# Performance work log

Measured on AMD Instinct MI355X. Metric: run time of the kernel, lower is better.

## Reference

```python
import jax, jax.numpy as jnp
import numpy as np

N_NODES = 100000
IN_DIM = 128
N_EDGES = 600000
HIDDEN = 128


def setup_inputs() -> dict:
    key = jax.random.key(0)
    k_z, k_e, k_w1, k_b1, k_w2, k_b2 = jax.random.split(key, 6)
    z = jax.random.normal(k_z, (N_NODES, IN_DIM), dtype=jnp.float32)
    edge_index = jax.random.randint(k_e, (2, N_EDGES), 0, N_NODES, dtype=jnp.int64)
    # torch.nn.Linear weights: W has shape (out, in), y = x @ W.T + b
    lim1 = 1.0 / np.sqrt(2 * IN_DIM)
    W1 = jax.random.uniform(k_w1, (HIDDEN, 2 * IN_DIM), jnp.float32, -lim1, lim1)
    b1 = jax.random.uniform(k_b1, (HIDDEN,), jnp.float32, -lim1, lim1)
    lim2 = 1.0 / np.sqrt(HIDDEN)
    W2 = jax.random.uniform(k_w2, (1, HIDDEN), jnp.float32, -lim2, lim2)
    b2 = jax.random.uniform(k_b2, (1,), jnp.float32, -lim2, lim2)
    return {"z": z, "edge_index": edge_index, "W1": W1, "b1": b1, "W2": W2, "b2": b2}


def reference(z, edge_index, W1, b1, W2, b2):
    src, dst = edge_index[0], edge_index[1]
    pair = jnp.concatenate([z[src], z[dst]], axis=1)        # [E, 2*in_dim]
    h = jax.nn.relu(pair @ W1.T + b1)                        # [E, 128]
    out = (h @ W2.T + b2).squeeze(-1)                        # [E]
    return out
```

## Files before the change

kernel.cpp:

```cpp
#include <hip/hip_runtime.h>

#define IN_DIM 128
#define NCOL   256

typedef __bf16 bfx8 __attribute__((ext_vector_type(8)));
typedef __bf16 bfx4 __attribute__((ext_vector_type(4)));
typedef float  f32x4 __attribute__((ext_vector_type(4)));

__device__ __forceinline__ int swz(int x) { return x ^ (((x >> 9) & 7) << 4); }

__global__ __launch_bounds__(256, 2) void gemm_mfma(
    const float* __restrict__ z, const float* __restrict__ W1,
    const float* __restrict__ b1, __bf16* __restrict__ UV, int nchunks)
{
    __shared__ float abuf[2][32 * IN_DIM];

    const int tid  = threadIdx.x;
    const int wave = tid >> 6;
    const int lane = tid & 63;
    const int l15  = lane & 15;
    const int q    = lane >> 4;
    const int n0   = wave * 64;

    bfx8  bfrag[4][4];
    f32x4 bias[4];
#pragma unroll
    for (int nt = 0; nt < 4; ++nt) {
        const int n = n0 + nt * 16 + l15;
        const float* src = (n < 128) ? (W1 + (size_t)n * 256)
                                     : (W1 + (size_t)(n - 128) * 256 + 128);
#pragma unroll
        for (int kk = 0; kk < 4; ++kk) {
            float4 f0 = *(const float4*)(src + kk * 32 + q * 8);
            float4 f1 = *(const float4*)(src + kk * 32 + q * 8 + 4);
            bfx8 b;
            b[0]=(__bf16)f0.x; b[1]=(__bf16)f0.y; b[2]=(__bf16)f0.z; b[3]=(__bf16)f0.w;
            b[4]=(__bf16)f1.x; b[5]=(__bf16)f1.y; b[6]=(__bf16)f1.z; b[7]=(__bf16)f1.w;
            bfrag[nt][kk] = b;
        }
        if (n0 + nt * 16 < 128) bias[nt] = *(const f32x4*)(b1 + n0 + nt * 16 + q * 4);
        else                    bias[nt] = (f32x4){0.f, 0.f, 0.f, 0.f};
    }

    auto STAGE = [&](int b, int cc) {
        const char* gbase = (const char*)(z + (size_t)cc * 32 * IN_DIM);
#pragma unroll
        for (int i = 0; i < 4; ++i) {
            const int seg  = (wave * 4 + i) << 10;
            const int loff = seg + lane * 16;
            __builtin_amdgcn_global_load_lds(
                (const __attribute__((address_space(1))) void*)(gbase + swz(loff)),
                (__attribute__((address_space(3))) void*)((char*)&abuf[b][0] + seg),
                16, 0, 0);
        }
    };

    int c = blockIdx.x;
    STAGE(0, c);
    __syncthreads();
    int cur = 0;

    for (; c < nchunks; c += gridDim.x) {
        const int cn = c + gridDim.x;
        if (cn < nchunks) STAGE(cur ^ 1, cn);

        const char* tb = (const char*)&abuf[cur][0];
        const int m0 = c * 32;

        f32x4 acc[2][4];
#pragma unroll
        for (int mt = 0; mt < 2; ++mt)
#pragma unroll
            for (int nt = 0; nt < 4; ++nt)
                acc[mt][nt] = (f32x4){0.f, 0.f, 0.f, 0.f};

#pragma unroll
        for (int kk = 0; kk < 4; ++kk) {
            bfx8 af[2];
#pragma unroll
            for (int mt = 0; mt < 2; ++mt) {
                const int r = mt * 16 + l15;
                const int o = r * 512 + kk * 128 + q * 32;
                f32x4 f0 = *(const f32x4*)(tb + swz(o));
                f32x4 f1 = *(const f32x4*)(tb + swz(o + 16));
                bfx8 a;
                a[0]=(__bf16)f0[0]; a[1]=(__bf16)f0[1]; a[2]=(__bf16)f0[2]; a[3]=(__bf16)f0[3];
                a[4]=(__bf16)f1[0]; a[5]=(__bf16)f1[1]; a[6]=(__bf16)f1[2]; a[7]=(__bf16)f1[3];
                af[mt] = a;
            }
#pragma unroll
            for (int mt = 0; mt < 2; ++mt)
#pragma unroll
                for (int nt = 0; nt < 4; ++nt)
                    acc[mt][nt] = __builtin_amdgcn_mfma_f32_16x16x32_bf16(
                        bfrag[nt][kk], af[mt], acc[mt][nt], 0, 0, 0);
        }

#pragma unroll
        for (int mt = 0; mt < 2; ++mt) {
            __bf16* dst = UV + (size_t)(m0 + mt * 16 + l15) * NCOL + n0 + q * 4;
#pragma unroll
            for (int nt = 0; nt < 4; ++nt) {
                bfx4 v;
#pragma unroll
                for (int r = 0; r < 4; ++r)
                    v[r] = (__bf16)(acc[mt][nt][r] + bias[nt][r]);
                *(bfx4*)(dst + nt * 16) = v;
            }
        }

        __syncthreads();
        cur ^= 1;
    }
}

__global__ __launch_bounds__(256) void edge_mlp(
    const __bf16* __restrict__ UV, const int* __restrict__ ei,
    const float* __restrict__ W2, const float* __restrict__ b2,
    float* __restrict__ out, int E)
{
    const int gt   = blockIdx.x * blockDim.x + threadIdx.x;
    const int lane = threadIdx.x & 15;
    const int g    = gt >> 4;
    const int e0   = g * 2;
    const int j0   = lane * 8;

    float ww[8];
    {
        float4 w0 = *(const float4*)(W2 + j0);
        float4 w1 = *(const float4*)(W2 + j0 + 4);
        ww[0] = w0.x; ww[1] = w0.y; ww[2] = w0.z; ww[3] = w0.w;
        ww[4] = w1.x; ww[5] = w1.y; ww[6] = w1.z; ww[7] = w1.w;
    }

    if (e0 >= E) return;

    const int2 srcp = *(const int2*)(ei + e0);
    const int2 dstp = *(const int2*)(ei + E + e0);

    bfx8 u0 = *(const bfx8*)(UV + (size_t)srcp.x * NCOL + j0);
    bfx8 v0 = *(const bfx8*)(UV + (size_t)dstp.x * NCOL + 128 + j0);
    bfx8 u1 = *(const bfx8*)(UV + (size_t)srcp.y * NCOL + j0);
    bfx8 v1 = *(const bfx8*)(UV + (size_t)dstp.y * NCOL + 128 + j0);

    float s0 = 0.f, s1 = 0.f;
#pragma unroll
    for (int i = 0; i < 8; ++i) {
        float h0 = (float)u0[i] + (float)v0[i];
        float h1 = (float)u1[i] + (float)v1[i];
        s0 = fmaf(fmaxf(h0, 0.f), ww[i], s0);
        s1 = fmaf(fmaxf(h1, 0.f), ww[i], s1);
    }

#pragma unroll
    for (int d = 1; d < 16; d <<= 1) {
        s0 += __shfl_xor(s0, d);
        s1 += __shfl_xor(s1, d);
    }

    if (lane == 0) {
        float bb = b2[0];
        *(float2*)(out + e0) = make_float2(s0 + bb, s1 + bb);
    }
}

extern "C" void kernel_launch(void* const* d_in, const int* in_sizes, int n_in,
                              void* d_out, int out_size, void* d_ws, size_t ws_size,
                              hipStream_t stream)
{
    const float* z  = (const float*)d_in[0];
    const int*   ei = (const int*)d_in[1];
    const float* W1 = (const float*)d_in[2];
    const float* b1 = (const float*)d_in[3];
    const float* W2 = (const float*)d_in[4];
    const float* b2 = (const float*)d_in[5];
    float* out = (float*)d_out;

    const int M = in_sizes[0] / IN_DIM;
    const int E = in_sizes[1] / 2;

    __bf16* UV = (__bf16*)d_ws;

    const int nchunks = M / 32;
    gemm_mfma<<<512, 256, 0, stream>>>(z, W1, b1, UV, nchunks);

    int groups  = (E + 1) / 2;
    int eblocks = (groups * 16 + 255) / 256;
    edge_mlp<<<eblocks, 256, 0, stream>>>(UV, ei, W2, b2, out, E);
}
```

Measured before the change: 154.4 us.

## Deepen GEMM LDS pipeline to four stages with explicit vmcnt waits

Raises the z-tile staging ring from double to quadruple buffering (three chunks in flight) and swaps __syncthreads for manual s_waitcnt vmcnt counts plus raw s_barrier, so compute waits only on the chunk it needs. LDS reads move to inline ds_read_b128 asm issued together before the MFMA loop. LDS use doubles to 64KB per block, which may limit occupancy at two blocks per CU. The hand-counted vmcnt values are fragile because they also count the UV global stores.

Result: no change. 151.5 us (-1.9%).

```diff
diff --git a/kernel.cpp b/kernel.cpp
--- a/kernel.cpp
+++ b/kernel.cpp
@@ -1,11 +1,14 @@
 #include <hip/hip_runtime.h>
+#include <stdint.h>
 
 #define IN_DIM 128
 #define NCOL   256
+#define CHUNK_B (32 * IN_DIM * 4)
 
 typedef __bf16 bfx8 __attribute__((ext_vector_type(8)));
 typedef __bf16 bfx4 __attribute__((ext_vector_type(4)));
 typedef float  f32x4 __attribute__((ext_vector_type(4)));
+typedef __attribute__((address_space(3))) void lds_void;
 
 __device__ __forceinline__ int swz(int x) { return x ^ (((x >> 9) & 7) << 4); }
 
@@ -13,7 +16,7 @@
     const float* __restrict__ z, const float* __restrict__ W1,
     const float* __restrict__ b1, __bf16* __restrict__ UV, int nchunks)
 {
-    __shared__ float abuf[2][32 * IN_DIM];
+    __shared__ float abuf[4][32 * IN_DIM];
 
     const int tid  = threadIdx.x;
     const int wave = tid >> 6;
@@ -42,6 +45,8 @@
         else                    bias[nt] = (f32x4){0.f, 0.f, 0.f, 0.f};
     }
 
+    const uint32_t lds0 = (uint32_t)(uintptr_t)(lds_void*)&abuf[0][0];
+
     auto STAGE = [&](int b, int cc) {
         const char* gbase = (const char*)(z + (size_t)cc * 32 * IN_DIM);
 #pragma unroll
@@ -50,22 +55,46 @@
             const int loff = seg + lane * 16;
             __builtin_amdgcn_global_load_lds(
                 (const __attribute__((address_space(1))) void*)(gbase + swz(loff)),
-                (__attribute__((address_space(3))) void*)((char*)&abuf[b][0] + seg),
+                (lds_void*)((char*)&abuf[b][0] + seg),
                 16, 0, 0);
         }
     };
 
-    int c = blockIdx.x;
-    STAGE(0, c);
-    __syncthreads();
-    int cur = 0;
-
-    for (; c < nchunks; c += gridDim.x) {
-        const int cn = c + gridDim.x;
-        if (cn < nchunks) STAGE(cur ^ 1, cn);
-
-        const char* tb = (const char*)&abuf[cur][0];
-        const int m0 = c * 32;
+    const int T = (nchunks - blockIdx.x + gridDim.x - 1) / gridDim.x;
+
+    STAGE(0, blockIdx.x);
+    STAGE(1, blockIdx.x + gridDim.x);
+    STAGE(2, blockIdx.x + 2 * gridDim.x);
+
+    for (int i = 0; i < T; ++i) {
+        const int c  = blockIdx.x + i * gridDim.x;
+        const bool st = (i + 3 < T);
+        if (st) STAGE((i + 3) & 3, c + 3 * gridDim.x);
+
+        if      (i == 0) asm volatile("s_waitcnt vmcnt(12)" ::: "memory");
+        else if (i == 1) asm volatile("s_waitcnt vmcnt(20)" ::: "memory");
+        else if (i == 2) asm volatile("s_waitcnt vmcnt(28)" ::: "memory");
+        else if (st)     asm volatile("s_waitcnt vmcnt(36)" ::: "memory");
+        else             asm volatile("s_waitcnt vmcnt(8)"  ::: "memory");
+        __builtin_amdgcn_s_barrier();
+        asm volatile("" ::: "memory");
+
+        const uint32_t tb = lds0 + (uint32_t)((i & 3) * CHUNK_B);
+
+        f32x4 rf[2][4][2];
+#pragma unroll
+        for (int mt = 0; mt < 2; ++mt)
+#pragma unroll
+            for (int kk = 0; kk < 4; ++kk)
+#pragma unroll
+                for (int h = 0; h < 2; ++h) {
+                    const int o = (mt * 16 + l15) * 512 + kk * 128 + q * 32 + h * 16;
+                    asm volatile("ds_read_b128 %0, %1"
+                                 : "=v"(rf[mt][kk][h])
+                                 : "v"(tb + (uint32_t)swz(o)));
+                }
+        asm volatile("s_waitcnt lgkmcnt(0)" ::: "memory");
+        __builtin_amdgcn_sched_barrier(0);
 
         f32x4 acc[2][4];
 #pragma unroll
@@ -79,10 +108,7 @@
             bfx8 af[2];
 #pragma unroll
             for (int mt = 0; mt < 2; ++mt) {
-                const int r = mt * 16 + l15;
-                const int o = r * 512 + kk * 128 + q * 32;
-                f32x4 f0 = *(const f32x4*)(tb + swz(o));
-                f32x4 f1 = *(const f32x4*)(tb + swz(o + 16));
+                f32x4 f0 = rf[mt][kk][0], f1 = rf[mt][kk][1];
                 bfx8 a;
                 a[0]=(__bf16)f0[0]; a[1]=(__bf16)f0[1]; a[2]=(__bf16)f0[2]; a[3]=(__bf16)f0[3];
                 a[4]=(__bf16)f1[0]; a[5]=(__bf16)f1[1]; a[6]=(__bf16)f1[2]; a[7]=(__bf16)f1[3];
@@ -96,6 +122,7 @@
                         bfrag[nt][kk], af[mt], acc[mt][nt], 0, 0, 0);
         }
 
+        const int m0 = c * 32;
 #pragma unroll
         for (int mt = 0; mt < 2; ++mt) {
             __bf16* dst = UV + (size_t)(m0 + mt * 16 + l15) * NCOL + n0 + q * 4;
@@ -109,8 +136,9 @@
             }
         }
 
-        __syncthreads();
-        cur ^= 1;
+        asm volatile("" ::: "memory");
+        __builtin_amdgcn_s_barrier();
+        asm volatile("" ::: "memory");
     }
 }
 
```
